# Kernel tuning notes

Hardware: AMD Instinct MI355X
Metric: run time of the kernel (lower is better)

Reference implementation:

```python
import jax, jax.numpy as jnp
import numpy as np

N_NODES = 100000
N_EDGES = 1600000
D_IN = 128
D_HID = 16
N_CLASSES = 40


def _glorot(key, shape):
    lim = float(np.sqrt(6.0 / (shape[0] + shape[1])))
    return jax.random.uniform(key, shape, jnp.float32, -lim, lim)


def setup_inputs() -> dict:
    key = jax.random.key(0)
    ks = jax.random.split(key, 8)
    x = jax.random.normal(ks[0], (N_NODES, D_IN), dtype=jnp.float32)
    edge_index = jax.random.randint(ks[1], (2, N_EDGES), 0, N_NODES, dtype=jnp.int64)
    return {
        "x": x,
        "edge_index": edge_index,
        # conv1: SAGEConv(D_IN, D_HID): lin_l (on aggregated, with bias), lin_r (on root, no bias)
        "W1l": _glorot(ks[2], (D_IN, D_HID)),
        "b1": jnp.zeros((D_HID,), jnp.float32),
        "W1r": _glorot(ks[3], (D_IN, D_HID)),
        # conv2: SAGEConv(D_HID, N_CLASSES)
        "W2l": _glorot(ks[4], (D_HID, N_CLASSES)),
        "b2": jnp.zeros((N_CLASSES,), jnp.float32),
        "W2r": _glorot(ks[5], (D_HID, N_CLASSES)),
    }


def _sage_conv(x, src, dst, Wl, bl, Wr, num_nodes):
    # mean aggregation of source-node features into destination nodes
    summed = jax.ops.segment_sum(x[src], dst, num_segments=num_nodes)  # [N, D]
    cnt = jax.ops.segment_sum(jnp.ones_like(dst, dtype=x.dtype), dst, num_segments=num_nodes)
    agg = summed / jnp.maximum(cnt, 1.0)[:, None]
    return agg @ Wl + bl + x @ Wr


def reference(x, edge_index, W1l, b1, W1r, W2l, b2, W2r):
    src, dst = edge_index[0], edge_index[1]
    n = x.shape[0]
    h = jax.nn.relu(_sage_conv(x, src, dst, W1l, b1, W1r, n))
    # F.dropout with training=self.training; module evaluated in eval mode -> identity
    out = _sage_conv(h, src, dst, W2l, b2, W2r, n)
    return jax.nn.log_softmax(out, axis=1)
```

## Files before the change

### kernel.cpp

```cpp
#include <hip/hip_runtime.h>
#include <math.h>

typedef _Float16 f16;

constexpr int NN   = 100000;
constexpr int DIN  = 128;
constexpr int DH   = 16;
constexpr int NC   = 40;
constexpr int CAP  = 48;
constexpr int NB   = (NN + 127) / 128;
constexpr int BC   = 2816;
constexpr int BSTR = 16;

static_assert(NN % 8 == 0, "agg grids assume NN % 8 == 0");

template <bool VEC4>
__global__ __launch_bounds__(1024)
void k_pp(const int* __restrict__ src, const int* __restrict__ dst, int E, int PBp,
          int* __restrict__ bcur, int* __restrict__ part,
          const float* __restrict__ x,
          const float* __restrict__ W1l, const float* __restrict__ W1r,
          f16* __restrict__ p1h, float* __restrict__ p1r)
{
    __shared__ int lh[NB];
    __shared__ int lbase[NB];
    int t = threadIdx.x;
    if ((int)blockIdx.x < PBp) {
        for (int i = t; i < NB; i += 1024) lh[i] = 0;
        __syncthreads();
        long base = (long)blockIdx.x * 8192;
        int pk[8], bk[8], rk[8];
        if (VEC4 && base + 8192 <= (long)E) {
            const int4* s4 = (const int4*)(src + base) + t * 2;
            const int4* d4 = (const int4*)(dst + base) + t * 2;
            int4 sa = s4[0], sb = s4[1];
            int4 da = d4[0], db = d4[1];
            int ss[8] = {sa.x, sa.y, sa.z, sa.w, sb.x, sb.y, sb.z, sb.w};
            int dd[8] = {da.x, da.y, da.z, da.w, db.x, db.y, db.z, db.w};
            #pragma unroll
            for (int i = 0; i < 8; ++i) {
                bk[i] = dd[i] >> 7;
                pk[i] = (ss[i] << 7) | (dd[i] & 127);
                rk[i] = atomicAdd(&lh[bk[i]], 1);
            }
        } else {
            #pragma unroll
            for (int i = 0; i < 8; ++i) {
                long e = base + (long)t * 8 + i;
                if (e < E) {
                    int s = src[e], d = dst[e];
                    bk[i] = d >> 7;
                    pk[i] = (s << 7) | (d & 127);
                    rk[i] = atomicAdd(&lh[bk[i]], 1);
                } else bk[i] = -1;
            }
        }
        __syncthreads();
        for (int i = t; i < NB; i += 1024)
            lbase[i] = lh[i] ? atomicAdd(&bcur[i * BSTR], lh[i]) : 0;
        __syncthreads();
        #pragma unroll
        for (int i = 0; i < 8; ++i) {
            if (bk[i] >= 0) {
                int idx = lbase[bk[i]] + rk[i];
                if (idx < BC) part[(long)bk[i] * BC + idx] = pk[i];
            }
        }
        return;
    }
    int bp = (int)blockIdx.x - PBp;
    int w  = t >> 6;
    int halfu = __builtin_amdgcn_readfirstlane(w & 1);
    long n = (long)bp * 512 + ((long)(w >> 1) << 6) + (t & 63);
    if (n >= NN) return;
    const float4* xr = (const float4*)(x + n * DIN);
    const float*  W  = halfu ? W1r : W1l;
    float acc[DH];
    #pragma unroll
    for (int j = 0; j < DH; ++j) acc[j] = 0.f;
    #pragma unroll 8
    for (int k4 = 0; k4 < 32; ++k4) {
        float4 v = xr[k4];
        const float* wr = W + k4 * 4 * DH;
        #pragma unroll
        for (int j = 0; j < DH; ++j) {
            acc[j] = fmaf(v.x, wr[j],          acc[j]);
            acc[j] = fmaf(v.y, wr[DH + j],     acc[j]);
            acc[j] = fmaf(v.z, wr[2 * DH + j], acc[j]);
            acc[j] = fmaf(v.w, wr[3 * DH + j], acc[j]);
        }
    }
    if (halfu == 0) {
        union { f16 f[16]; uint4 q[2]; } u;
        #pragma unroll
        for (int j = 0; j < DH; ++j) u.f[j] = (f16)acc[j];
        uint4* po = (uint4*)(p1h + n * DH);
        po[0] = u.q[0]; po[1] = u.q[1];
    } else {
        float4* pr = (float4*)(p1r + n * DH);
        pr[0] = make_float4(acc[0],  acc[1],  acc[2],  acc[3]);
        pr[1] = make_float4(acc[4],  acc[5],  acc[6],  acc[7]);
        pr[2] = make_float4(acc[8],  acc[9],  acc[10], acc[11]);
        pr[3] = make_float4(acc[12], acc[13], acc[14], acc[15]);
    }
}

__global__ __launch_bounds__(512)
void k_ba1(const int* __restrict__ bcur, const int* __restrict__ part,
           const uint4* __restrict__ g4, const float4* __restrict__ p1r4,
           const float* __restrict__ b1,
           int* __restrict__ cnt, int* __restrict__ col, uint4* __restrict__ h4)
{
    __shared__ int scol[128 * CAP];
    __shared__ int cur[128];
    int t = threadIdx.x, b = blockIdx.x;
    if (t < 128) cur[t] = 0;
    __syncthreads();
    long base = (long)b * BC;
    int ne = min(bcur[b * BSTR], BC);
    for (int e = t; e < ne; e += 512) {
        int pk = part[base + e];
        int dl = pk & 127;
        int r  = atomicAdd(&cur[dl], 1);
        if (r < CAP) scol[dl * CAP + r] = pk >> 7;
    }
    __syncthreads();
    if (t < 128) {
        int node = (b << 7) + t;
        if (node < NN) cnt[node] = cur[t];
    }
    int* gcol = col + (long)b * 128 * CAP;
    for (int i = t; i < 128 * CAP; i += 512) gcol[i] = scol[i];

    int nl = t >> 2, dh = (t >> 1) & 1, ng = t & 1;
    int node = (b << 7) + nl;
    int degf = cur[nl];
    int deg  = min(degf, CAP);
    const int* cb = scol + nl * CAP;
    float a[8];
    #pragma unroll
    for (int j = 0; j < 8; ++j) a[j] = 0.f;
    int i = ng;
    for (; i + 6 < deg; i += 8) {
        int s0 = cb[i], s1 = cb[i+2], s2 = cb[i+4], s3 = cb[i+6];
        uint4 v0 = g4[(long)s0*2+dh], v1 = g4[(long)s1*2+dh],
              v2 = g4[(long)s2*2+dh], v3 = g4[(long)s3*2+dh];
        const f16 *p0=(const f16*)&v0, *p1=(const f16*)&v1,
                  *p2=(const f16*)&v2, *p3=(const f16*)&v3;
        #pragma unroll
        for (int j = 0; j < 8; ++j)
            a[j] += (float)p0[j] + (float)p1[j] + (float)p2[j] + (float)p3[j];
    }
    for (; i < deg; i += 2) {
        int s = cb[i];
        uint4 v = g4[(long)s*2+dh];
        const f16* p = (const f16*)&v;
        #pragma unroll
        for (int j = 0; j < 8; ++j) a[j] += (float)p[j];
    }
    #pragma unroll
    for (int j = 0; j < 8; ++j) a[j] += __shfl_xor(a[j], 1);
    if (ng == 0 && node < NN) {
        float inv = 1.0f / fmaxf((float)degf, 1.0f);
        float4 bl = ((const float4*)b1)[dh*2+0];
        float4 bh = ((const float4*)b1)[dh*2+1];
        float4 rl = p1r4[(long)node*4 + dh*2+0];
        float4 rh = p1r4[(long)node*4 + dh*2+1];
        float bb[8] = {bl.x,bl.y,bl.z,bl.w, bh.x,bh.y,bh.z,bh.w};
        float rr[8] = {rl.x,rl.y,rl.z,rl.w, rh.x,rh.y,rh.z,rh.w};
        union { f16 f[8]; uint4 u; } o;
        #pragma unroll
        for (int j = 0; j < 8; ++j)
            o.f[j] = (f16)fmaxf(fmaf(a[j], inv, bb[j] + rr[j]), 0.f);
        h4[(long)node*2+dh] = o.u;
    }
}

__global__ void k_agg2o(const int* __restrict__ cnt, const int* __restrict__ col,
                        const uint4* __restrict__ g4,
                        const float* __restrict__ W2l, const float* __restrict__ b2,
                        const float* __restrict__ W2r, float* __restrict__ out)
{
    __shared__ float sW[2 * DH * NC + NC];
    __shared__ float sA[32][DH + 1];
    __shared__ float sH[32][DH + 1];
    int t = threadIdx.x;
    for (int i = t; i < DH * NC; i += 256) {
        sW[i]           = W2l[i];
        sW[DH * NC + i] = W2r[i];
    }
    if (t < NC) sW[2 * DH * NC + t] = b2[t];

    int lane = t & 63;
    int wv   = (blockIdx.x * 256 + t) >> 6;
    int n    = wv * 8 + (lane >> 3);
    int dh   = (lane >> 2) & 1;
    int ng   = lane & 3;
    int nl2  = t >> 3;
    int degf = cnt[n];
    int deg  = min(degf, CAP);
    const int* cb = col + (long)n * CAP;
    float a[8];
    #pragma unroll
    for (int j = 0; j < 8; ++j) a[j] = 0.f;
    int i = ng;
    for (; i + 12 < deg; i += 16) {
        int s0 = cb[i], s1 = cb[i+4], s2 = cb[i+8], s3 = cb[i+12];
        uint4 v0 = g4[(long)s0*2+dh], v1 = g4[(long)s1*2+dh],
              v2 = g4[(long)s2*2+dh], v3 = g4[(long)s3*2+dh];
        const f16 *p0=(const f16*)&v0, *p1=(const f16*)&v1,
                  *p2=(const f16*)&v2, *p3=(const f16*)&v3;
        #pragma unroll
        for (int j = 0; j < 8; ++j)
            a[j] += (float)p0[j] + (float)p1[j] + (float)p2[j] + (float)p3[j];
    }
    for (; i < deg; i += 4) {
        int s = cb[i];
        uint4 v = g4[(long)s*2+dh];
        const f16* p = (const f16*)&v;
        #pragma unroll
        for (int j = 0; j < 8; ++j) a[j] += (float)p[j];
    }
    #pragma unroll
    for (int j = 0; j < 8; ++j) {
        a[j] += __shfl_xor(a[j], 1);
        a[j] += __shfl_xor(a[j], 2);
    }
    if (ng == 0) {
        float inv = 1.0f / fmaxf((float)degf, 1.0f);
        #pragma unroll
        for (int j = 0; j < 8; ++j) sA[nl2][dh*8+j] = a[j] * inv;
    } else if (ng == 1) {
        uint4 hv4 = g4[(long)n*2+dh];
        const f16* hp = (const f16*)&hv4;
        #pragma unroll
        for (int j = 0; j < 8; ++j) sH[nl2][dh*8+j] = (float)hp[j];
    }
    __syncthreads();

    float av[DH], hv[DH];
    #pragma unroll
    for (int j = 0; j < DH; ++j) { av[j] = sA[nl2][j]; hv[j] = sH[nl2][j]; }
    int lane8 = t & 7;
    float o[5];
    #pragma unroll
    for (int j = 0; j < 5; ++j) {
        int c = lane8 + 8 * j;
        float acc = sW[2 * DH * NC + c];
        #pragma unroll
        for (int k = 0; k < DH; ++k) {
            acc = fmaf(av[k], sW[k * NC + c],           acc);
            acc = fmaf(hv[k], sW[DH * NC + k * NC + c], acc);
        }
        o[j] = acc;
    }
    float mx = o[0];
    #pragma unroll
    for (int j = 1; j < 5; ++j) mx = fmaxf(mx, o[j]);
    #pragma unroll
    for (int m = 1; m <= 4; m <<= 1) mx = fmaxf(mx, __shfl_xor(mx, m));
    float s = 0.f;
    #pragma unroll
    for (int j = 0; j < 5; ++j) s += __expf(o[j] - mx);
    #pragma unroll
    for (int m = 1; m <= 4; m <<= 1) s += __shfl_xor(s, m);
    float lg = mx + __logf(s);
    float* op = out + (long)n * NC;
    #pragma unroll
    for (int j = 0; j < 5; ++j) op[lane8 + 8 * j] = o[j] - lg;
}


extern "C" void kernel_launch(void* const* d_in, const int* in_sizes, int n_in,
                              void* d_out, int out_size, void* d_ws, size_t ws_size,
                              hipStream_t stream) {
    const float* x   = (const float*)d_in[0];
    const int*   ei  = (const int*)d_in[1];
    const float* W1l = (const float*)d_in[2];
    const float* b1  = (const float*)d_in[3];
    const float* W1r = (const float*)d_in[4];
    const float* W2l = (const float*)d_in[5];
    const float* b2  = (const float*)d_in[6];
    const float* W2r = (const float*)d_in[7];
    float* out = (float*)d_out;

    const int E = in_sizes[1] / 2;
    const int* src = ei;
    const int* dst = ei + E;

    int* bcur = (int*)d_ws;
    int* cnt  = bcur + 12544;
    int* col  = cnt + NN;
    int* part = col + (long)NB * 128 * CAP;
    float* p1r = (float*)(part + (long)NB * BC);
    f16*   p1h = (f16*)(p1r + (long)NN * DH);
    f16*   h   = p1h + (long)NN * DH;

    hipMemsetAsync(bcur, 0, NB * BSTR * sizeof(int), stream);

    const int PBp = (E + 8191) / 8192;
    const int PBj = (NN + 511) / 512;
    if ((E & 3) == 0)
        k_pp<true ><<<PBp + PBj, 1024, 0, stream>>>(src, dst, E, PBp, bcur, part,
                                                    x, W1l, W1r, p1h, p1r);
    else
        k_pp<false><<<PBp + PBj, 1024, 0, stream>>>(src, dst, E, PBp, bcur, part,
                                                    x, W1l, W1r, p1h, p1r);

    k_ba1  <<<NB, 512, 0, stream>>>(bcur, part, (const uint4*)p1h,
                                    (const float4*)p1r, b1, cnt, col, (uint4*)h);
    k_agg2o<<<(NN + 31) / 32, 256, 0, stream>>>(cnt, col, (const uint4*)h,
                                                W2l, b2, W2r, out);
}
```

Before: 182.7 us.

## Split fused partition/projection kernel and split-K the layer-1 projection

Separates the edge partitioning and the x@W1 projection, which previously shared one launch via block-index dispatch, into two kernels. The new projection kernel uses 256-thread blocks over 64 nodes and splits the 128-wide K dimension in half across thread groups, reducing the partial sums through shared memory. The goal is more parallelism and shorter per-thread serial FMA chains on the memory-bound projection. In exchange it adds a separate launch and loses the overlap between partitioning and projection that the fused launch allowed.

```diff
diff --git a/kernel.cpp b/kernel.cpp
--- a/kernel.cpp
+++ b/kernel.cpp
@@ -16,72 +16,75 @@
 
 template <bool VEC4>
 __global__ __launch_bounds__(1024)
-void k_pp(const int* __restrict__ src, const int* __restrict__ dst, int E, int PBp,
-          int* __restrict__ bcur, int* __restrict__ part,
-          const float* __restrict__ x,
-          const float* __restrict__ W1l, const float* __restrict__ W1r,
-          f16* __restrict__ p1h, float* __restrict__ p1r)
+void k_part(const int* __restrict__ src, const int* __restrict__ dst, int E,
+            int* __restrict__ bcur, int* __restrict__ part)
 {
     __shared__ int lh[NB];
     __shared__ int lbase[NB];
     int t = threadIdx.x;
-    if ((int)blockIdx.x < PBp) {
-        for (int i = t; i < NB; i += 1024) lh[i] = 0;
-        __syncthreads();
-        long base = (long)blockIdx.x * 8192;
-        int pk[8], bk[8], rk[8];
-        if (VEC4 && base + 8192 <= (long)E) {
-            const int4* s4 = (const int4*)(src + base) + t * 2;
-            const int4* d4 = (const int4*)(dst + base) + t * 2;
-            int4 sa = s4[0], sb = s4[1];
-            int4 da = d4[0], db = d4[1];
-            int ss[8] = {sa.x, sa.y, sa.z, sa.w, sb.x, sb.y, sb.z, sb.w};
-            int dd[8] = {da.x, da.y, da.z, da.w, db.x, db.y, db.z, db.w};
-            #pragma unroll
-            for (int i = 0; i < 8; ++i) {
-                bk[i] = dd[i] >> 7;
-                pk[i] = (ss[i] << 7) | (dd[i] & 127);
+    for (int i = t; i < NB; i += 1024) lh[i] = 0;
+    __syncthreads();
+    long base = (long)blockIdx.x * 8192;
+    int pk[8], bk[8], rk[8];
+    if (VEC4 && base + 8192 <= (long)E) {
+        const int4* s4 = (const int4*)(src + base) + t * 2;
+        const int4* d4 = (const int4*)(dst + base) + t * 2;
+        int4 sa = s4[0], sb = s4[1];
+        int4 da = d4[0], db = d4[1];
+        int ss[8] = {sa.x, sa.y, sa.z, sa.w, sb.x, sb.y, sb.z, sb.w};
+        int dd[8] = {da.x, da.y, da.z, da.w, db.x, db.y, db.z, db.w};
+        #pragma unroll
+        for (int i = 0; i < 8; ++i) {
+            bk[i] = dd[i] >> 7;
+            pk[i] = (ss[i] << 7) | (dd[i] & 127);
+            rk[i] = atomicAdd(&lh[bk[i]], 1);
+        }
+    } else {
+        #pragma unroll
+        for (int i = 0; i < 8; ++i) {
+            long e = base + (long)t * 8 + i;
+            if (e < E) {
+                int s = src[e], d = dst[e];
+                bk[i] = d >> 7;
+                pk[i] = (s << 7) | (d & 127);
                 rk[i] = atomicAdd(&lh[bk[i]], 1);
-            }
-        } else {
-            #pragma unroll
-            for (int i = 0; i < 8; ++i) {
-                long e = base + (long)t * 8 + i;
-                if (e < E) {
-                    int s = src[e], d = dst[e];
-                    bk[i] = d >> 7;
-                    pk[i] = (s << 7) | (d & 127);
-                    rk[i] = atomicAdd(&lh[bk[i]], 1);
-                } else bk[i] = -1;
-            }
-        }
-        __syncthreads();
-        for (int i = t; i < NB; i += 1024)
-            lbase[i] = lh[i] ? atomicAdd(&bcur[i * BSTR], lh[i]) : 0;
-        __syncthreads();
-        #pragma unroll
-        for (int i = 0; i < 8; ++i) {
-            if (bk[i] >= 0) {
-                int idx = lbase[bk[i]] + rk[i];
-                if (idx < BC) part[(long)bk[i] * BC + idx] = pk[i];
-            }
-        }
-        return;
-    }
-    int bp = (int)blockIdx.x - PBp;
-    int w  = t >> 6;
-    int halfu = __builtin_amdgcn_readfirstlane(w & 1);
-    long n = (long)bp * 512 + ((long)(w >> 1) << 6) + (t & 63);
-    if (n >= NN) return;
-    const float4* xr = (const float4*)(x + n * DIN);
-    const float*  W  = halfu ? W1r : W1l;
+            } else bk[i] = -1;
+        }
+    }
+    __syncthreads();
+    for (int i = t; i < NB; i += 1024)
+        lbase[i] = lh[i] ? atomicAdd(&bcur[i * BSTR], lh[i]) : 0;
+    __syncthreads();
+    #pragma unroll
+    for (int i = 0; i < 8; ++i) {
+        if (bk[i] >= 0) {
+            int idx = lbase[bk[i]] + rk[i];
+            if (idx < BC) part[(long)bk[i] * BC + idx] = pk[i];
+        }
+    }
+}
+
+__global__ void k_proj(const float* __restrict__ x,
+                       const float* __restrict__ W1l, const float* __restrict__ W1r,
+                       f16* __restrict__ p1h, float* __restrict__ p1r)
+{
+    __shared__ float ps[2][64][DH + 1];
+    int t  = threadIdx.x;
+    int nl = t & 63;
+    int halfu = __builtin_amdgcn_readfirstlane((t >> 6) & 1);
+    int khu   = __builtin_amdgcn_readfirstlane(t >> 7);
+    long n  = (long)blockIdx.x * 64 + nl;
+    long ncl = n < NN ? n : NN - 1;
+    const float4* xr = (const float4*)(x + ncl * DIN + khu * 64);
+    const float*  Wk = (halfu ? W1r : W1l) + khu * 64 * DH;
+
     float acc[DH];
     #pragma unroll
     for (int j = 0; j < DH; ++j) acc[j] = 0.f;
-    #pragma unroll 8
-    for (int k4 = 0; k4 < 32; ++k4) {
+    #pragma unroll
+    for (int k4 = 0; k4 < 16; ++k4) {
         float4 v = xr[k4];
-        const float* wr = W + k4 * 4 * DH;
+        const float* wr = Wk + k4 * 4 * DH;
         #pragma unroll
         for (int j = 0; j < DH; ++j) {
             acc[j] = fmaf(v.x, wr[j],          acc[j]);
@@ -90,18 +93,27 @@
             acc[j] = fmaf(v.w, wr[3 * DH + j], acc[j]);
         }
     }
-    if (halfu == 0) {
-        union { f16 f[16]; uint4 q[2]; } u;
-        #pragma unroll
-        for (int j = 0; j < DH; ++j) u.f[j] = (f16)acc[j];
-        uint4* po = (uint4*)(p1h + n * DH);
-        po[0] = u.q[0]; po[1] = u.q[1];
-    } else {
-        float4* pr = (float4*)(p1r + n * DH);
-        pr[0] = make_float4(acc[0],  acc[1],  acc[2],  acc[3]);
-        pr[1] = make_float4(acc[4],  acc[5],  acc[6],  acc[7]);
-        pr[2] = make_float4(acc[8],  acc[9],  acc[10], acc[11]);
-        pr[3] = make_float4(acc[12], acc[13], acc[14], acc[15]);
+    if (khu) {
+        #pragma unroll
+        for (int j = 0; j < DH; ++j) ps[halfu][nl][j] = acc[j];
+    }
+    __syncthreads();
+    if (!khu && n < NN) {
+        #pragma unroll
+        for (int j = 0; j < DH; ++j) acc[j] += ps[halfu][nl][j];
+        if (halfu == 0) {
+            union { f16 f[16]; uint4 q[2]; } u;
+            #pragma unroll
+            for (int j = 0; j < DH; ++j) u.f[j] = (f16)acc[j];
+            uint4* po = (uint4*)(p1h + n * DH);
+            po[0] = u.q[0]; po[1] = u.q[1];
+        } else {
+            float4* pr = (float4*)(p1r + n * DH);
+            pr[0] = make_float4(acc[0],  acc[1],  acc[2],  acc[3]);
+            pr[1] = make_float4(acc[4],  acc[5],  acc[6],  acc[7]);
+            pr[2] = make_float4(acc[8],  acc[9],  acc[10], acc[11]);
+            pr[3] = make_float4(acc[12], acc[13], acc[14], acc[15]);
+        }
     }
 }
 
@@ -298,14 +310,12 @@
 
     hipMemsetAsync(bcur, 0, NB * BSTR * sizeof(int), stream);
 
-    const int PBp = (E + 8191) / 8192;
-    const int PBj = (NN + 511) / 512;
     if ((E & 3) == 0)
-        k_pp<true ><<<PBp + PBj, 1024, 0, stream>>>(src, dst, E, PBp, bcur, part,
-                                                    x, W1l, W1r, p1h, p1r);
+        k_part<true ><<<(E + 8191) / 8192, 1024, 0, stream>>>(src, dst, E, bcur, part);
     else
-        k_pp<false><<<PBp + PBj, 1024, 0, stream>>>(src, dst, E, PBp, bcur, part,
-                                                    x, W1l, W1r, p1h, p1r);
+        k_part<false><<<(E + 8191) / 8192, 1024, 0, stream>>>(src, dst, E, bcur, part);
+
+    k_proj <<<(NN + 63) / 64, 256, 0, stream>>>(x, W1l, W1r, p1h, p1r);
 
     k_ba1  <<<NB, 512, 0, stream>>>(bcur, part, (const uint4*)p1h,
                                     (const float4*)p1r, b1, cnt, col, (uint4*)h);
```

Result: no change. 184.3 us (+0.9%).
